# Performance work log

Hardware: AMD Instinct MI355X
Metric: run time of the kernel (lower is better)

The kernel has to match this reference:

```python
import jax, jax.numpy as jnp
import numpy as np

D_MODEL = 1024
N_HEADS = 16
HEAD_DIM = D_MODEL // N_HEADS
D_FF = 4096
SEQ = 2048
BATCH = 4
THETA = 10000.0
EPS = 1e-5


def rmsnorm(x, w, eps=EPS):
    xf = x.astype(jnp.float32)
    var = jnp.mean(xf * xf, axis=-1, keepdims=True) + eps
    return (xf * jax.lax.rsqrt(var) * w).astype(x.dtype)


def rope_tables(head_dim, max_len, theta):
    freqs = 1.0 / theta ** (jnp.arange(0, head_dim, 2, dtype=jnp.float32) / head_dim)
    t = jnp.arange(max_len, dtype=jnp.float32)
    ang = jnp.outer(t, freqs)  # [T, Hs/2]
    return jnp.cos(ang), jnp.sin(ang)


def apply_rope(x, cos, sin):
    # x: [B, H, T, Hs]; cos/sin: [T, Hs/2] (broadcast over B, H)
    x1 = x[..., 0::2]
    x2 = x[..., 1::2]
    o1 = x1 * cos - x2 * sin
    o2 = x1 * sin + x2 * cos
    return jnp.stack([o1, o2], axis=-1).reshape(x.shape).astype(x.dtype)


def setup_inputs() -> dict:
    key = jax.random.key(0)
    ks = jax.random.split(key, 12)
    s = 0.02
    return {
        "x": jax.random.normal(ks[0], (BATCH, SEQ, D_MODEL), dtype=jnp.float32),
        "token_positions": jnp.arange(SEQ, dtype=jnp.int32),
        "ln1_w": jnp.ones((D_MODEL,), dtype=jnp.float32),
        "q_w": jax.random.normal(ks[1], (D_MODEL, D_MODEL), dtype=jnp.float32) * s,
        "k_w": jax.random.normal(ks[2], (D_MODEL, D_MODEL), dtype=jnp.float32) * s,
        "v_w": jax.random.normal(ks[3], (D_MODEL, D_MODEL), dtype=jnp.float32) * s,
        "o_w": jax.random.normal(ks[4], (D_MODEL, D_MODEL), dtype=jnp.float32) * s,
        "ln2_w": jnp.ones((D_MODEL,), dtype=jnp.float32),
        "w1": jax.random.normal(ks[5], (D_FF, D_MODEL), dtype=jnp.float32) * s,
        "w2": jax.random.normal(ks[6], (D_MODEL, D_FF), dtype=jnp.float32) * s,
        "w3": jax.random.normal(ks[7], (D_FF, D_MODEL), dtype=jnp.float32) * s,
    }


def reference(x, token_positions, ln1_w, q_w, k_w, v_w, o_w, ln2_w, w1, w2, w3):
    B, T, D = x.shape
    cos_full, sin_full = rope_tables(HEAD_DIM, SEQ, THETA)
    cos = cos_full[token_positions]
    sin = sin_full[token_positions]

    # --- attention sublayer ---
    h = rmsnorm(x, ln1_w)
    q = jnp.einsum('btd,od->bto', h, q_w)
    k = jnp.einsum('btd,od->bto', h, k_w)
    v = jnp.einsum('btd,od->bto', h, v_w)
    # [B, T, D] -> [B, H, T, Hs]
    def split_heads(t_):
        return t_.reshape(B, T, N_HEADS, HEAD_DIM).transpose(0, 2, 1, 3)
    xq, xk, xv = split_heads(q), split_heads(k), split_heads(v)
    xq = apply_rope(xq, cos, sin)
    xk = apply_rope(xk, cos, sin)

    scores = jnp.einsum('bhqd,bhkd->bhqk', xq, xk) / jnp.sqrt(jnp.float32(HEAD_DIM))
    causal = jnp.tril(jnp.ones((T, T), dtype=bool))
    scores = jnp.where(causal, scores, jnp.float32(-jnp.inf))
    attn = jax.nn.softmax(scores, axis=-1)
    ctx = jnp.einsum('bhqk,bhkd->bhqd', attn, xv)
    ctx = ctx.transpose(0, 2, 1, 3).reshape(B, T, D)
    x = x + jnp.einsum('btd,od->bto', ctx, o_w)

    # --- SwiGLU FFN sublayer ---
    h2 = rmsnorm(x, ln2_w)
    a = jnp.einsum('btd,fd->btf', h2, w1)
    g = jnp.einsum('btd,fd->btf', h2, w3)
    ff = jnp.einsum('btf,df->btd', a * jax.nn.sigmoid(a) * g, w2)
    return x + ff
```

## Files before the change

### kernel.cpp

```cpp
#include <hip/hip_runtime.h>
#include <hip/hip_bf16.h>

#define D_MODEL 1024
#define N_HEADS 16
#define HEAD_DIM 64
#define D_FF 4096
#define SEQ 2048
#define BATCH 4
#define NTOK (BATCH*SEQ)

typedef __attribute__((ext_vector_type(4))) float  f32x4;
typedef __attribute__((ext_vector_type(8))) short  s16x8;
typedef __attribute__((ext_vector_type(4))) unsigned short u16x4;

typedef __attribute__((address_space(1))) const unsigned int gas_u32;
typedef __attribute__((address_space(3))) unsigned int las_u32;

__device__ __forceinline__ void gload_lds16(const void* g, void* l) {
  __builtin_amdgcn_global_load_lds((gas_u32*)g, (las_u32*)l, 16, 0, 0);
}

__device__ __forceinline__ float bf2f(unsigned short u) {
  union { unsigned int i; float f; } v; v.i = ((unsigned int)u) << 16; return v.f;
}
__device__ __forceinline__ unsigned short f2bf(float f) {
  union { float f; unsigned int i; } v; v.f = f;
  return (unsigned short)((v.i + 0x7fffu + ((v.i >> 16) & 1u)) >> 16);
}

__global__ __launch_bounds__(256) void cvt_k(const float* __restrict__ in,
                                             unsigned short* __restrict__ out, int n) {
  for (long i = ((long)blockIdx.x*256 + threadIdx.x)*4; i < n; i += (long)gridDim.x*1024) {
    f32x4 v = *(const f32x4*)&in[i];
    u16x4 o;
    #pragma unroll
    for (int c=0;c<4;c++) o[c] = f2bf(v[c]);
    *(u16x4*)&out[i] = o;
  }
}

__global__ __launch_bounds__(256) void rope_tables_k(const int* __restrict__ pos,
                                                     float* __restrict__ cosT,
                                                     float* __restrict__ sinT) {
  int idx = blockIdx.x*256 + threadIdx.x;
  int t = idx >> 5, i = idx & 31;
  float p  = (float)pos[t];
  float fr = powf(10000.0f, -(float)i * (1.0f/32.0f));
  float ang = p * fr;
  cosT[idx] = cosf(ang);
  sinT[idx] = sinf(ang);
}

__global__ __launch_bounds__(256) void rmsnorm_k(const float* __restrict__ x,
                                                 const float* __restrict__ wgt,
                                                 unsigned short* __restrict__ out) {
  const long row = blockIdx.x;
  const int t = threadIdx.x;
  f32x4 v = *(const f32x4*)&x[row*D_MODEL + t*4];
  float ss = v[0]*v[0] + v[1]*v[1] + v[2]*v[2] + v[3]*v[3];
  #pragma unroll
  for (int off=1; off<64; off<<=1) ss += __shfl_xor(ss, off, 64);
  __shared__ float red[4];
  if ((t & 63) == 0) red[t >> 6] = ss;
  __syncthreads();
  float tot = red[0] + red[1] + red[2] + red[3];
  float inv = rsqrtf(tot * (1.0f/D_MODEL) + 1e-5f);
  f32x4 wv = *(const f32x4*)&wgt[t*4];
  u16x4 o;
  #pragma unroll
  for (int c=0;c<4;c++) o[c] = f2bf(v[c] * inv * wv[c]);
  *(u16x4*)&out[row*D_MODEL + t*4] = o;
}

__global__ __launch_bounds__(256) void rope_k(unsigned short* __restrict__ q,
                                              unsigned short* __restrict__ k,
                                              const float* __restrict__ cosT,
                                              const float* __restrict__ sinT) {
  long idx = (long)blockIdx.x*256 + threadIdx.x;
  int ig = (int)(idx & 7);
  long th = idx >> 3;
  int h = (int)(th & 15);
  long bt = th >> 4;
  int t = (int)(bt & (SEQ-1));
  long off = bt*D_MODEL + h*HEAD_DIM + ig*8;
  f32x4 cs = *(const f32x4*)&cosT[t*32 + ig*4];
  f32x4 sn = *(const f32x4*)&sinT[t*32 + ig*4];
  s16x8 qv = *(const s16x8*)&q[off];
  s16x8 kv = *(const s16x8*)&k[off];
  s16x8 qo, ko;
  #pragma unroll
  for (int p=0;p<4;p++) {
    float q1 = bf2f((unsigned short)qv[2*p]), q2 = bf2f((unsigned short)qv[2*p+1]);
    qo[2*p]   = (short)f2bf(q1*cs[p] - q2*sn[p]);
    qo[2*p+1] = (short)f2bf(q1*sn[p] + q2*cs[p]);
    float k1 = bf2f((unsigned short)kv[2*p]), k2 = bf2f((unsigned short)kv[2*p+1]);
    ko[2*p]   = (short)f2bf(k1*cs[p] - k2*sn[p]);
    ko[2*p+1] = (short)f2bf(k1*sn[p] + k2*cs[p]);
  }
  *(s16x8*)&q[off] = qo;
  *(s16x8*)&k[off] = ko;
}

template<int EPI>
__global__ __launch_bounds__(256) void gemm_bt(const unsigned short* __restrict__ A,
                                               const unsigned short* __restrict__ W,
                                               unsigned short* __restrict__ Cb,
                                               float* __restrict__ Cf,
                                               const float* __restrict__ resid,
                                               int M, int N, int K) {
  __shared__ __align__(16) unsigned short As[128*64];
  __shared__ __align__(16) unsigned short Bs[128*64];

  const int nwg = gridDim.x * gridDim.y;
  int orig = blockIdx.y * gridDim.x + blockIdx.x;
  int swz = orig;
  if ((nwg & 7) == 0) {
    int cpx = nwg >> 3;
    swz = (orig & 7) * cpx + (orig >> 3);
  }
  const int bx = swz % gridDim.x;
  const int by = swz / gridDim.x;

  const int tid = threadIdx.x;
  const int w  = tid >> 6;
  const int l  = tid & 63;
  const int lr = l & 15;
  const int lg = l >> 4;
  const int wm = (w >> 1) * 64;
  const int wn = (w & 1) * 64;

  const long rowA0 = (long)by * 128;
  const long rowB0 = (long)bx * 128;

  f32x4 acc[4][4] = {};

  for (int kt = 0; kt < K; kt += 64) {
    #pragma unroll
    for (int it = 0; it < 4; ++it) {
      int chunk = it*256 + tid;
      int row = chunk >> 3;
      int csw = (chunk & 7) ^ (row & 7);
      gload_lds16(&A[(rowA0 + row)*(long)K + kt + csw*8], &As[chunk*8]);
    }
    #pragma unroll
    for (int it = 0; it < 4; ++it) {
      int chunk = it*256 + tid;
      int row = chunk >> 3;
      int csw = (chunk & 7) ^ (row & 7);
      gload_lds16(&W[(rowB0 + row)*(long)K + kt + csw*8], &Bs[chunk*8]);
    }
    __syncthreads();

    s16x8 af[2][4], bfv[2][4];
    #pragma unroll
    for (int m=0;m<4;m++) {
      int row = wm + m*16 + lr;
      #pragma unroll
      for (int kk=0;kk<2;kk++) {
        int sw = (kk*4+lg) ^ (row & 7);
        af[kk][m] = *(const s16x8*)&As[row*64 + sw*8];
      }
    }
    #pragma unroll
    for (int n=0;n<4;n++) {
      int row = wn + n*16 + lr;
      #pragma unroll
      for (int kk=0;kk<2;kk++) {
        int sw = (kk*4+lg) ^ (row & 7);
        bfv[kk][n] = *(const s16x8*)&Bs[row*64 + sw*8];
      }
    }
    #pragma unroll
    for (int kk=0;kk<2;kk++)
      #pragma unroll
      for (int m=0;m<4;m++)
        #pragma unroll
        for (int n=0;n<4;n++)
          acc[m][n] = __builtin_amdgcn_mfma_f32_16x16x32_bf16(af[kk][m], bfv[kk][n], acc[m][n], 0,0,0);
    __syncthreads();
  }

  #pragma unroll
  for (int m=0;m<4;m++)
    #pragma unroll
    for (int n=0;n<4;n++)
      #pragma unroll
      for (int r=0;r<4;r++) {
        long row = rowA0 + wm + m*16 + lg*4 + r;
        long col = rowB0 + wn + n*16 + lr;
        float val = acc[m][n][r];
        if constexpr (EPI == 0) {
          Cb[row*(long)N + col] = f2bf(val);
        } else {
          Cf[row*(long)N + col] = resid[row*(long)N + col] + val;
        }
      }
}

__global__ __launch_bounds__(256) void attn_k(const unsigned short* __restrict__ Q,
                                              const unsigned short* __restrict__ K,
                                              const unsigned short* __restrict__ V,
                                              unsigned short* __restrict__ O) {
  const int bh = blockIdx.x;
  const int b = bh >> 4;
  const int h = bh & 15;
  const int tid = threadIdx.x;
  const int w  = tid >> 6;
  const int l  = tid & 63;
  const int lr = l & 15;
  const int lg = l >> 4;

  __shared__ __align__(16) unsigned short Vs[2][64*64];
  __shared__ __align__(16) unsigned short Ps[4][16][72];

  const int skv = tid >> 2;
  const int sd0 = (tid & 3) * 16;
  const long vbase = (long)(b*SEQ)*D_MODEL + h*HEAD_DIM;

  for (int pass = 0; pass < 2; ++pass) {
    const int qt = pass ? 31 - blockIdx.y : blockIdx.y;
    const int q0 = qt * 64;
    const int ntile = qt + 1;

    const long rowQ = (long)(b*SEQ + q0 + w*16 + lr);
    s16x8 qf0 = *(const s16x8*)&Q[rowQ*D_MODEL + h*HEAD_DIM + lg*8];
    s16x8 qf1 = *(const s16x8*)&Q[rowQ*D_MODEL + h*HEAD_DIM + 32 + lg*8];

    float mi[4], li[4];
    f32x4 oa[4] = {};
    #pragma unroll
    for (int r=0;r<4;r++) { mi[r] = -1e30f; li[r] = 0.f; }

    {
      const unsigned short* src = &V[vbase + (long)skv*D_MODEL + sd0];
      s16x8 v0 = *(const s16x8*)&src[0];
      s16x8 v1 = *(const s16x8*)&src[8];
      #pragma unroll
      for (int i=0;i<16;i++) {
        int d = sd0 + i;
        int key = (d&7) ^ ((d>>3)&7);
        int c = (skv>>3) ^ key;
        Vs[0][d*64 + c*8 + (skv&7)] = (unsigned short)(i<8 ? v0[i] : v1[i-8]);
      }
    }
    __syncthreads();

    for (int t=0; t<ntile; ++t) {
      const int kv0 = t*64;
      const int cur = t & 1;
      const int nb  = cur ^ 1;
      const bool more = (t+1 < ntile);

      s16x8 v0, v1;
      if (more) {
        const unsigned short* src = &V[vbase + (long)((t+1)*64 + skv)*D_MODEL + sd0];
        v0 = *(const s16x8*)&src[0];
        v1 = *(const s16x8*)&src[8];
      }

      f32x4 s[4];
      #pragma unroll
      for (int j=0;j<4;j++) {
        const long rowK = (long)(b*SEQ + kv0 + j*16 + lr);
        s16x8 kf0 = *(const s16x8*)&K[rowK*D_MODEL + h*HEAD_DIM + lg*8];
        s16x8 kf1 = *(const s16x8*)&K[rowK*D_MODEL + h*HEAD_DIM + 32 + lg*8];
        f32x4 acc = {};
        acc = __builtin_amdgcn_mfma_f32_16x16x32_bf16(qf0, kf0, acc, 0,0,0);
        acc = __builtin_amdgcn_mfma_f32_16x16x32_bf16(qf1, kf1, acc, 0,0,0);
        s[j] = acc * 0.125f;
      }
      if (t == ntile-1) {
        #pragma unroll
        for (int j=0;j<4;j++)
          #pragma unroll
          for (int r=0;r<4;r++) {
            int kvg = kv0 + j*16 + lr;
            int qg  = q0 + w*16 + lg*4 + r;
            if (kvg > qg) s[j][r] = -1e30f;
          }
      }
      float al[4];
      #pragma unroll
      for (int r=0;r<4;r++) {
        float v = fmaxf(fmaxf(s[0][r], s[1][r]), fmaxf(s[2][r], s[3][r]));
        #pragma unroll
        for (int off=1; off<16; off<<=1) v = fmaxf(v, __shfl_xor(v, off, 64));
        float mn = fmaxf(mi[r], v);
        al[r] = __expf(mi[r] - mn);
        mi[r] = mn;
      }
      #pragma unroll
      for (int j=0;j<4;j++)
        #pragma unroll
        for (int r=0;r<4;r++) s[j][r] = __expf(s[j][r] - mi[r]);
      #pragma unroll
      for (int r=0;r<4;r++) {
        float v = s[0][r]+s[1][r]+s[2][r]+s[3][r];
        #pragma unroll
        for (int off=1; off<16; off<<=1) v += __shfl_xor(v, off, 64);
        li[r] = li[r]*al[r] + v;
      }
      #pragma unroll
      for (int d=0;d<4;d++)
        #pragma unroll
        for (int r=0;r<4;r++) oa[d][r] *= al[r];
      #pragma unroll
      for (int j=0;j<4;j++)
        #pragma unroll
        for (int r=0;r<4;r++)
          Ps[w][lg*4+r][j*16+lr] = f2bf(s[j][r]);

      if (more) {
        #pragma unroll
        for (int i=0;i<16;i++) {
          int d = sd0 + i;
          int key = (d&7) ^ ((d>>3)&7);
          int c = (skv>>3) ^ key;
          Vs[nb][d*64 + c*8 + (skv&7)] = (unsigned short)(i<8 ? v0[i] : v1[i-8]);
        }
      }

      #pragma unroll
      for (int kk=0;kk<2;kk++) {
        s16x8 pa = *(const s16x8*)&Ps[w][lr][kk*32+lg*8];
        #pragma unroll
        for (int d=0;d<4;d++) {
          int row = d*16 + lr;
          int key = (row&7) ^ ((row>>3)&7);
          int c = (kk*4+lg) ^ key;
          s16x8 vb = *(const s16x8*)&Vs[cur][row*64 + c*8];
          oa[d] = __builtin_amdgcn_mfma_f32_16x16x32_bf16(pa, vb, oa[d], 0,0,0);
        }
      }
      __syncthreads();
    }

    #pragma unroll
    for (int d=0;d<4;d++)
      #pragma unroll
      for (int r=0;r<4;r++) {
        long row = (long)(b*SEQ + q0 + w*16 + lg*4 + r);
        O[row*D_MODEL + h*HEAD_DIM + d*16 + lr] = f2bf(oa[d][r] / li[r]);
      }
  }
}

__global__ __launch_bounds__(256) void swiglu_k(unsigned short* __restrict__ a,
                                                const unsigned short* __restrict__ g) {
  long i = ((long)blockIdx.x*256 + threadIdx.x)*8;
  s16x8 av = *(const s16x8*)&a[i];
  s16x8 gv = *(const s16x8*)&g[i];
  s16x8 o;
  #pragma unroll
  for (int c=0;c<8;c++) {
    float xx = bf2f((unsigned short)av[c]);
    float yy = bf2f((unsigned short)gv[c]);
    float sg = 1.0f / (1.0f + __expf(-xx));
    o[c] = (short)f2bf(xx * sg * yy);
  }
  *(s16x8*)&a[i] = o;
}

extern "C" void kernel_launch(void* const* d_in, const int* in_sizes, int n_in,
                              void* d_out, int out_size, void* d_ws, size_t ws_size,
                              hipStream_t stream) {
  (void)in_sizes; (void)n_in; (void)out_size; (void)ws_size;
  const float* x    = (const float*)d_in[0];
  const int*   tpos = (const int*)d_in[1];
  const float* ln1  = (const float*)d_in[2];
  const float* qw   = (const float*)d_in[3];
  const float* kw   = (const float*)d_in[4];
  const float* vw   = (const float*)d_in[5];
  const float* ow   = (const float*)d_in[6];
  const float* ln2  = (const float*)d_in[7];
  const float* w1   = (const float*)d_in[8];
  const float* w2   = (const float*)d_in[9];
  const float* w3   = (const float*)d_in[10];
  float* out = (float*)d_out;

  char* ws = (char*)d_ws;
  size_t off = 0;
  auto nalloc = [&](size_t b) { void* p = ws + off; off += (b + 255) & ~(size_t)255; return p; };

  unsigned short* wqb = (unsigned short*)nalloc((size_t)D_MODEL*D_MODEL*2);
  unsigned short* wkb = (unsigned short*)nalloc((size_t)D_MODEL*D_MODEL*2);
  unsigned short* wvb = (unsigned short*)nalloc((size_t)D_MODEL*D_MODEL*2);
  unsigned short* wob = (unsigned short*)nalloc((size_t)D_MODEL*D_MODEL*2);
  unsigned short* w1b = (unsigned short*)nalloc((size_t)D_FF*D_MODEL*2);
  unsigned short* w3b = (unsigned short*)nalloc((size_t)D_FF*D_MODEL*2);
  unsigned short* w2b = (unsigned short*)nalloc((size_t)D_MODEL*D_FF*2);
  float* cosT = (float*)nalloc((size_t)SEQ*32*4);
  float* sinT = (float*)nalloc((size_t)SEQ*32*4);
  unsigned short* h    = (unsigned short*)nalloc((size_t)NTOK*D_MODEL*2);
  unsigned short* qb   = (unsigned short*)nalloc((size_t)NTOK*D_MODEL*2);
  unsigned short* kb   = (unsigned short*)nalloc((size_t)NTOK*D_MODEL*2);
  unsigned short* vb   = (unsigned short*)nalloc((size_t)NTOK*D_MODEL*2);
  unsigned short* ctxb = (unsigned short*)nalloc((size_t)NTOK*D_MODEL*2);
  float* x2 = (float*)nalloc((size_t)NTOK*D_MODEL*4);
  unsigned short* gbuf = (unsigned short*)nalloc((size_t)NTOK*D_FF*2);
  unsigned short* abuf = qb;

  cvt_k<<<1024,256,0,stream>>>(qw, wqb, D_MODEL*D_MODEL);
  cvt_k<<<1024,256,0,stream>>>(kw, wkb, D_MODEL*D_MODEL);
  cvt_k<<<1024,256,0,stream>>>(vw, wvb, D_MODEL*D_MODEL);
  cvt_k<<<1024,256,0,stream>>>(ow, wob, D_MODEL*D_MODEL);
  cvt_k<<<2048,256,0,stream>>>(w1, w1b, D_FF*D_MODEL);
  cvt_k<<<2048,256,0,stream>>>(w2, w2b, D_MODEL*D_FF);
  cvt_k<<<2048,256,0,stream>>>(w3, w3b, D_FF*D_MODEL);
  rope_tables_k<<<SEQ*32/256,256,0,stream>>>(tpos, cosT, sinT);

  rmsnorm_k<<<NTOK,256,0,stream>>>(x, ln1, h);
  gemm_bt<0><<<dim3(8,64),256,0,stream>>>(h, wqb, qb, nullptr, nullptr, NTOK, D_MODEL, D_MODEL);
  gemm_bt<0><<<dim3(8,64),256,0,stream>>>(h, wkb, kb, nullptr, nullptr, NTOK, D_MODEL, D_MODEL);
  gemm_bt<0><<<dim3(8,64),256,0,stream>>>(h, wvb, vb, nullptr, nullptr, NTOK, D_MODEL, D_MODEL);
  rope_k<<<4096,256,0,stream>>>(qb, kb, cosT, sinT);
  attn_k<<<dim3(64,16),256,0,stream>>>(qb, kb, vb, ctxb);
  gemm_bt<1><<<dim3(8,64),256,0,stream>>>(ctxb, wob, nullptr, x2, x, NTOK, D_MODEL, D_MODEL);

  rmsnorm_k<<<NTOK,256,0,stream>>>(x2, ln2, h);
  gemm_bt<0><<<dim3(32,64),256,0,stream>>>(h, w1b, abuf, nullptr, nullptr, NTOK, D_FF, D_MODEL);
  gemm_bt<0><<<dim3(32,64),256,0,stream>>>(h, w3b, gbuf, nullptr, nullptr, NTOK, D_FF, D_MODEL);
  swiglu_k<<<(long)NTOK*D_FF/8/256,256,0,stream>>>(abuf, gbuf);
  gemm_bt<1><<<dim3(8,64),256,0,stream>>>(abuf, w2b, nullptr, out, x2, NTOK, D_MODEL, D_FF);
}
```

Measured before the change: 719.2 us.

## Fuse QKV projection, stage K in LDS, restructure attention softmax, add double-buffered GEMM

Packs Q, K and V weights into one matrix so a single GEMM writes an interleaved QKV buffer, replacing three launches. RoPE now also folds the 1/sqrt(d) scale into Q. The attention kernel loads K tiles into swizzled, double-buffered LDS and computes the transposed score product so softmax reductions need fewer shuffles. It also swizzles the P buffer and raises wave priority around MFMA sections. A new double-buffered gemm_db kernel is introduced but used only for the w1 projection, and it doubles LDS use, which may lower occupancy.

After: 647.1 us. -10.0%, faster.

```diff
diff --git a/kernel.cpp b/kernel.cpp
--- a/kernel.cpp
+++ b/kernel.cpp
@@ -8,6 +8,7 @@
 #define SEQ 2048
 #define BATCH 4
 #define NTOK (BATCH*SEQ)
+#define QS 3072
 
 typedef __attribute__((ext_vector_type(4))) float  f32x4;
 typedef __attribute__((ext_vector_type(8))) short  s16x8;
@@ -72,8 +73,7 @@
   *(u16x4*)&out[row*D_MODEL + t*4] = o;
 }
 
-__global__ __launch_bounds__(256) void rope_k(unsigned short* __restrict__ q,
-                                              unsigned short* __restrict__ k,
+__global__ __launch_bounds__(256) void rope_k(unsigned short* __restrict__ qkv,
                                               const float* __restrict__ cosT,
                                               const float* __restrict__ sinT) {
   long idx = (long)blockIdx.x*256 + threadIdx.x;
@@ -82,23 +82,23 @@
   int h = (int)(th & 15);
   long bt = th >> 4;
   int t = (int)(bt & (SEQ-1));
-  long off = bt*D_MODEL + h*HEAD_DIM + ig*8;
+  long off = bt*QS + h*HEAD_DIM + ig*8;
   f32x4 cs = *(const f32x4*)&cosT[t*32 + ig*4];
   f32x4 sn = *(const f32x4*)&sinT[t*32 + ig*4];
-  s16x8 qv = *(const s16x8*)&q[off];
-  s16x8 kv = *(const s16x8*)&k[off];
+  s16x8 qv = *(const s16x8*)&qkv[off];
+  s16x8 kv = *(const s16x8*)&qkv[off + 1024];
   s16x8 qo, ko;
   #pragma unroll
   for (int p=0;p<4;p++) {
     float q1 = bf2f((unsigned short)qv[2*p]), q2 = bf2f((unsigned short)qv[2*p+1]);
-    qo[2*p]   = (short)f2bf(q1*cs[p] - q2*sn[p]);
-    qo[2*p+1] = (short)f2bf(q1*sn[p] + q2*cs[p]);
+    qo[2*p]   = (short)f2bf((q1*cs[p] - q2*sn[p]) * 0.125f);
+    qo[2*p+1] = (short)f2bf((q1*sn[p] + q2*cs[p]) * 0.125f);
     float k1 = bf2f((unsigned short)kv[2*p]), k2 = bf2f((unsigned short)kv[2*p+1]);
     ko[2*p]   = (short)f2bf(k1*cs[p] - k2*sn[p]);
     ko[2*p+1] = (short)f2bf(k1*sn[p] + k2*cs[p]);
   }
-  *(s16x8*)&q[off] = qo;
-  *(s16x8*)&k[off] = ko;
+  *(s16x8*)&qkv[off] = qo;
+  *(s16x8*)&qkv[off + 1024] = ko;
 }
 
 template<int EPI>
@@ -197,9 +197,111 @@
       }
 }
 
-__global__ __launch_bounds__(256) void attn_k(const unsigned short* __restrict__ Q,
-                                              const unsigned short* __restrict__ K,
-                                              const unsigned short* __restrict__ V,
+template<int EPI>
+__global__ __launch_bounds__(256) void gemm_db(const unsigned short* __restrict__ A,
+                                               const unsigned short* __restrict__ W,
+                                               unsigned short* __restrict__ Cb,
+                                               float* __restrict__ Cf,
+                                               const float* __restrict__ resid,
+                                               int M, int N, int K) {
+  __shared__ __align__(16) unsigned short As[2][128*64];
+  __shared__ __align__(16) unsigned short Bs[2][128*64];
+
+  const int nwg = gridDim.x * gridDim.y;
+  int orig = blockIdx.y * gridDim.x + blockIdx.x;
+  int swz = orig;
+  if ((nwg & 7) == 0) {
+    int cpx = nwg >> 3;
+    swz = (orig & 7) * cpx + (orig >> 3);
+  }
+  const int bx = swz % gridDim.x;
+  const int by = swz / gridDim.x;
+
+  const int tid = threadIdx.x;
+  const int w  = tid >> 6;
+  const int l  = tid & 63;
+  const int lr = l & 15;
+  const int lg = l >> 4;
+  const int wm = (w >> 1) * 64;
+  const int wn = (w & 1) * 64;
+
+  const long rowA0 = (long)by * 128;
+  const long rowB0 = (long)bx * 128;
+
+  f32x4 acc[4][4] = {};
+  const int nk = K >> 6;
+
+  #pragma unroll
+  for (int it = 0; it < 4; ++it) {
+    int chunk = it*256 + tid;
+    int row = chunk >> 3;
+    int csw = (chunk & 7) ^ (row & 7);
+    gload_lds16(&A[(rowA0 + row)*(long)K + csw*8], &As[0][chunk*8]);
+    gload_lds16(&W[(rowB0 + row)*(long)K + csw*8], &Bs[0][chunk*8]);
+  }
+  __syncthreads();
+
+  int cur = 0;
+  for (int ki = 0; ki < nk; ++ki) {
+    if (ki + 1 < nk) {
+      int kt = (ki + 1) << 6;
+      #pragma unroll
+      for (int it = 0; it < 4; ++it) {
+        int chunk = it*256 + tid;
+        int row = chunk >> 3;
+        int csw = (chunk & 7) ^ (row & 7);
+        gload_lds16(&A[(rowA0 + row)*(long)K + kt + csw*8], &As[cur^1][chunk*8]);
+        gload_lds16(&W[(rowB0 + row)*(long)K + kt + csw*8], &Bs[cur^1][chunk*8]);
+      }
+    }
+    s16x8 af[2][4], bfv[2][4];
+    #pragma unroll
+    for (int m=0;m<4;m++) {
+      int row = wm + m*16 + lr;
+      #pragma unroll
+      for (int kk=0;kk<2;kk++) {
+        int sw = (kk*4+lg) ^ (row & 7);
+        af[kk][m] = *(const s16x8*)&As[cur][row*64 + sw*8];
+      }
+    }
+    #pragma unroll
+    for (int n=0;n<4;n++) {
+      int row = wn + n*16 + lr;
+      #pragma unroll
+      for (int kk=0;kk<2;kk++) {
+        int sw = (kk*4+lg) ^ (row & 7);
+        bfv[kk][n] = *(const s16x8*)&Bs[cur][row*64 + sw*8];
+      }
+    }
+    #pragma unroll
+    for (int kk=0;kk<2;kk++)
+      #pragma unroll
+      for (int m=0;m<4;m++)
+        #pragma unroll
+        for (int n=0;n<4;n++)
+          acc[m][n] = __builtin_amdgcn_mfma_f32_16x16x32_bf16(af[kk][m], bfv[kk][n], acc[m][n], 0,0,0);
+    __syncthreads();
+    cur ^= 1;
+  }
+
+  #pragma unroll
+  for (int m=0;m<4;m++)
+    #pragma unroll
+    for (int n=0;n<4;n++)
+      #pragma unroll
+      for (int r=0;r<4;r++) {
+        long row = rowA0 + wm + m*16 + lg*4 + r;
+        long col = rowB0 + wn + n*16 + lr;
+        float val = acc[m][n][r];
+        if constexpr (EPI == 0) {
+          Cb[row*(long)N + col] = f2bf(val);
+        } else {
+          Cf[row*(long)N + col] = resid[row*(long)N + col] + val;
+        }
+      }
+}
+
+__global__ __launch_bounds__(256) void attn_k(const unsigned short* __restrict__ QKV,
                                               unsigned short* __restrict__ O) {
   const int bh = blockIdx.x;
   const int b = bh >> 4;
@@ -210,29 +312,39 @@
   const int lr = l & 15;
   const int lg = l >> 4;
 
+  const unsigned short* Qp = QKV;
+  const unsigned short* Kp = QKV + 1024;
+  const unsigned short* Vp = QKV + 2048;
+
+  __shared__ __align__(16) unsigned short Ks[2][64*64];
   __shared__ __align__(16) unsigned short Vs[2][64*64];
-  __shared__ __align__(16) unsigned short Ps[4][16][72];
+  __shared__ __align__(16) unsigned short Ps[4][16][64];
 
   const int skv = tid >> 2;
   const int sd0 = (tid & 3) * 16;
-  const long vbase = (long)(b*SEQ)*D_MODEL + h*HEAD_DIM;
+  const long hbase = (long)(b*SEQ)*QS + h*HEAD_DIM;
 
   for (int pass = 0; pass < 2; ++pass) {
-    const int qt = pass ? 31 - blockIdx.y : blockIdx.y;
+    const int qt = pass ? 31 - (int)blockIdx.y : (int)blockIdx.y;
     const int q0 = qt * 64;
     const int ntile = qt + 1;
 
     const long rowQ = (long)(b*SEQ + q0 + w*16 + lr);
-    s16x8 qf0 = *(const s16x8*)&Q[rowQ*D_MODEL + h*HEAD_DIM + lg*8];
-    s16x8 qf1 = *(const s16x8*)&Q[rowQ*D_MODEL + h*HEAD_DIM + 32 + lg*8];
-
-    float mi[4], li[4];
+    s16x8 qf0 = *(const s16x8*)&Qp[rowQ*QS + h*HEAD_DIM + lg*8];
+    s16x8 qf1 = *(const s16x8*)&Qp[rowQ*QS + h*HEAD_DIM + 32 + lg*8];
+
+    float mi = -1e30f, li = 0.f;
     f32x4 oa[4] = {};
-    #pragma unroll
-    for (int r=0;r<4;r++) { mi[r] = -1e30f; li[r] = 0.f; }
-
+
+    #pragma unroll
+    for (int it=0; it<2; ++it) {
+      int chunk = it*256 + tid;
+      int row = chunk >> 3;
+      int csw = (chunk & 7) ^ (row & 7);
+      gload_lds16(&Kp[hbase + (long)row*QS + csw*8], &Ks[0][chunk*8]);
+    }
     {
-      const unsigned short* src = &V[vbase + (long)skv*D_MODEL + sd0];
+      const unsigned short* src = &Vp[hbase + (long)skv*QS + sd0];
       s16x8 v0 = *(const s16x8*)&src[0];
       s16x8 v1 = *(const s16x8*)&src[8];
       #pragma unroll
@@ -253,62 +365,79 @@
 
       s16x8 v0, v1;
       if (more) {
-        const unsigned short* src = &V[vbase + (long)((t+1)*64 + skv)*D_MODEL + sd0];
+        #pragma unroll
+        for (int it=0; it<2; ++it) {
+          int chunk = it*256 + tid;
+          int row = chunk >> 3;
+          int csw = (chunk & 7) ^ (row & 7);
+          gload_lds16(&Kp[hbase + (long)(kv0 + 64 + row)*QS + csw*8], &Ks[nb][chunk*8]);
+        }
+        const unsigned short* src = &Vp[hbase + (long)(kv0 + 64 + skv)*QS + sd0];
         v0 = *(const s16x8*)&src[0];
         v1 = *(const s16x8*)&src[8];
       }
 
       f32x4 s[4];
+      __builtin_amdgcn_s_setprio(1);
       #pragma unroll
       for (int j=0;j<4;j++) {
-        const long rowK = (long)(b*SEQ + kv0 + j*16 + lr);
-        s16x8 kf0 = *(const s16x8*)&K[rowK*D_MODEL + h*HEAD_DIM + lg*8];
-        s16x8 kf1 = *(const s16x8*)&K[rowK*D_MODEL + h*HEAD_DIM + 32 + lg*8];
+        int krow = j*16 + lr;
+        s16x8 kf0 = *(const s16x8*)&Ks[cur][krow*64 + ((lg)     ^ (krow&7))*8];
+        s16x8 kf1 = *(const s16x8*)&Ks[cur][krow*64 + ((4 + lg) ^ (krow&7))*8];
         f32x4 acc = {};
-        acc = __builtin_amdgcn_mfma_f32_16x16x32_bf16(qf0, kf0, acc, 0,0,0);
-        acc = __builtin_amdgcn_mfma_f32_16x16x32_bf16(qf1, kf1, acc, 0,0,0);
-        s[j] = acc * 0.125f;
-      }
+        acc = __builtin_amdgcn_mfma_f32_16x16x32_bf16(kf0, qf0, acc, 0,0,0);
+        acc = __builtin_amdgcn_mfma_f32_16x16x32_bf16(kf1, qf1, acc, 0,0,0);
+        s[j] = acc;
+      }
+      __builtin_amdgcn_s_setprio(0);
+
       if (t == ntile-1) {
         #pragma unroll
         for (int j=0;j<4;j++)
           #pragma unroll
-          for (int r=0;r<4;r++) {
-            int kvg = kv0 + j*16 + lr;
-            int qg  = q0 + w*16 + lg*4 + r;
-            if (kvg > qg) s[j][r] = -1e30f;
-          }
-      }
-      float al[4];
-      #pragma unroll
-      for (int r=0;r<4;r++) {
-        float v = fmaxf(fmaxf(s[0][r], s[1][r]), fmaxf(s[2][r], s[3][r]));
-        #pragma unroll
-        for (int off=1; off<16; off<<=1) v = fmaxf(v, __shfl_xor(v, off, 64));
-        float mn = fmaxf(mi[r], v);
-        al[r] = __expf(mi[r] - mn);
-        mi[r] = mn;
-      }
+          for (int r=0;r<4;r++)
+            if (kv0 + j*16 + lg*4 + r > q0 + w*16 + lr) s[j][r] = -1e30f;
+      }
+
+      float pmax = s[0][0];
       #pragma unroll
       for (int j=0;j<4;j++)
         #pragma unroll
-        for (int r=0;r<4;r++) s[j][r] = __expf(s[j][r] - mi[r]);
-      #pragma unroll
-      for (int r=0;r<4;r++) {
-        float v = s[0][r]+s[1][r]+s[2][r]+s[3][r];
-        #pragma unroll
-        for (int off=1; off<16; off<<=1) v += __shfl_xor(v, off, 64);
-        li[r] = li[r]*al[r] + v;
-      }
+        for (int r=0;r<4;r++) pmax = fmaxf(pmax, s[j][r]);
+      pmax = fmaxf(pmax, __shfl_xor(pmax, 16, 64));
+      pmax = fmaxf(pmax, __shfl_xor(pmax, 32, 64));
+      float mn = fmaxf(mi, pmax);
+      float al = __expf(mi - mn);
+      mi = mn;
+      float psum = 0.f;
+      #pragma unroll
+      for (int j=0;j<4;j++)
+        #pragma unroll
+        for (int r=0;r<4;r++) {
+          float p = __expf(s[j][r] - mn);
+          s[j][r] = p;
+          psum += p;
+        }
+      psum += __shfl_xor(psum, 16, 64);
+      psum += __shfl_xor(psum, 32, 64);
+      li = li*al + psum;
+
+      float alq[4];
+      #pragma unroll
+      for (int r=0;r<4;r++) alq[r] = __shfl(al, lg*4 + r, 64);
       #pragma unroll
       for (int d=0;d<4;d++)
         #pragma unroll
-        for (int r=0;r<4;r++) oa[d][r] *= al[r];
+        for (int r=0;r<4;r++) oa[d][r] *= alq[r];
+
       #pragma unroll
       for (int j=0;j<4;j++)
         #pragma unroll
-        for (int r=0;r<4;r++)
-          Ps[w][lg*4+r][j*16+lr] = f2bf(s[j][r]);
+        for (int r=0;r<4;r++) {
+          int k = j*16 + lg*4 + r;
+          int pos = ((k>>3) ^ (lr&7))*8 + (k&7);
+          Ps[w][lr][pos] = f2bf(s[j][r]);
+        }
 
       if (more) {
         #pragma unroll
@@ -320,27 +449,32 @@
         }
       }
 
+      __builtin_amdgcn_s_setprio(1);
       #pragma unroll
       for (int kk=0;kk<2;kk++) {
-        s16x8 pa = *(const s16x8*)&Ps[w][lr][kk*32+lg*8];
+        s16x8 pa = *(const s16x8*)&Ps[w][lr][((kk*4 + lg) ^ (lr&7))*8];
         #pragma unroll
         for (int d=0;d<4;d++) {
-          int row = d*16 + lr;
-          int key = (row&7) ^ ((row>>3)&7);
-          int c = (kk*4+lg) ^ key;
-          s16x8 vb = *(const s16x8*)&Vs[cur][row*64 + c*8];
+          int vrow = d*16 + lr;
+          int key = (vrow&7) ^ ((vrow>>3)&7);
+          int c = (kk*4 + lg) ^ key;
+          s16x8 vb = *(const s16x8*)&Vs[cur][vrow*64 + c*8];
           oa[d] = __builtin_amdgcn_mfma_f32_16x16x32_bf16(pa, vb, oa[d], 0,0,0);
         }
       }
+      __builtin_amdgcn_s_setprio(0);
       __syncthreads();
     }
 
+    float liq[4];
+    #pragma unroll
+    for (int r=0;r<4;r++) liq[r] = __shfl(li, lg*4 + r, 64);
     #pragma unroll
     for (int d=0;d<4;d++)
       #pragma unroll
       for (int r=0;r<4;r++) {
         long row = (long)(b*SEQ + q0 + w*16 + lg*4 + r);
-        O[row*D_MODEL + h*HEAD_DIM + d*16 + lr] = f2bf(oa[d][r] / li[r]);
+        O[row*D_MODEL + h*HEAD_DIM + d*16 + lr] = f2bf(oa[d][r] / liq[r]);
       }
   }
 }
@@ -382,44 +516,38 @@
   size_t off = 0;
   auto nalloc = [&](size_t b) { void* p = ws + off; off += (b + 255) & ~(size_t)255; return p; };
 
-  unsigned short* wqb = (unsigned short*)nalloc((size_t)D_MODEL*D_MODEL*2);
-  unsigned short* wkb = (unsigned short*)nalloc((size_t)D_MODEL*D_MODEL*2);
-  unsigned short* wvb = (unsigned short*)nalloc((size_t)D_MODEL*D_MODEL*2);
-  unsigned short* wob = (unsigned short*)nalloc((size_t)D_MODEL*D_MODEL*2);
-  unsigned short* w1b = (unsigned short*)nalloc((size_t)D_FF*D_MODEL*2);
-  unsigned short* w3b = (unsigned short*)nalloc((size_t)D_FF*D_MODEL*2);
-  unsigned short* w2b = (unsigned short*)nalloc((size_t)D_MODEL*D_FF*2);
+  unsigned short* wqkvb = (unsigned short*)nalloc((size_t)3072*D_MODEL*2);
+  unsigned short* wob   = (unsigned short*)nalloc((size_t)D_MODEL*D_MODEL*2);
+  unsigned short* w1b   = (unsigned short*)nalloc((size_t)D_FF*D_MODEL*2);
+  unsigned short* w3b   = (unsigned short*)nalloc((size_t)D_FF*D_MODEL*2);
+  unsigned short* w2b   = (unsigned short*)nalloc((size_t)D_MODEL*D_FF*2);
   float* cosT = (float*)nalloc((size_t)SEQ*32*4);
   float* sinT = (float*)nalloc((size_t)SEQ*32*4);
-  unsigned short* h    = (unsigned short*)nalloc((size_t)NTOK*D_MODEL*2);
-  unsigned short* qb   = (unsigned short*)nalloc((size_t)NTOK*D_MODEL*2);
-  unsigned short* kb   = (unsigned short*)nalloc((size_t)NTOK*D_MODEL*2);
-  unsigned short* vb   = (unsigned short*)nalloc((size_t)NTOK*D_MODEL*2);
+  unsigned short* hbuf = (unsigned short*)nalloc((size_t)NTOK*D_MODEL*2);
+  unsigned short* qkv  = (unsigned short*)nalloc((size_t)NTOK*QS*2);
   unsigned short* ctxb = (unsigned short*)nalloc((size_t)NTOK*D_MODEL*2);
   float* x2 = (float*)nalloc((size_t)NTOK*D_MODEL*4);
   unsigned short* gbuf = (unsigned short*)nalloc((size_t)NTOK*D_FF*2);
-  unsigned short* abuf = qb;
-
-  cvt_k<<<1024,256,0,stream>>>(qw, wqb, D_MODEL*D_MODEL);
-  cvt_k<<<1024,256,0,stream>>>(kw, wkb, D_MODEL*D_MODEL);
-  cvt_k<<<1024,256,0,stream>>>(vw, wvb, D_MODEL*D_MODEL);
+  unsigned short* abuf = qkv;
+
+  cvt_k<<<1024,256,0,stream>>>(qw, wqkvb,                 D_MODEL*D_MODEL);
+  cvt_k<<<1024,256,0,stream>>>(kw, wqkvb + 1024*D_MODEL,  D_MODEL*D_MODEL);
+  cvt_k<<<1024,256,0,stream>>>(vw, wqkvb + 2048*D_MODEL,  D_MODEL*D_MODEL);
   cvt_k<<<1024,256,0,stream>>>(ow, wob, D_MODEL*D_MODEL);
   cvt_k<<<2048,256,0,stream>>>(w1, w1b, D_FF*D_MODEL);
   cvt_k<<<2048,256,0,stream>>>(w2, w2b, D_MODEL*D_FF);
   cvt_k<<<2048,256,0,stream>>>(w3, w3b, D_FF*D_MODEL);
   rope_tables_k<<<SEQ*32/256,256,0,stream>>>(tpos, cosT, sinT);
 
-  rmsnorm_k<<<NTOK,256,0,stream>>>(x, ln1, h);
-  gemm_bt<0><<<dim3(8,64),256,0,stream>>>(h, wqb, qb, nullptr, nullptr, NTOK, D_MODEL, D_MODEL);
-  gemm_bt<0><<<dim3(8,64),256,0,stream>>>(h, wkb, kb, nullptr, nullptr, NTOK, D_MODEL, D_MODEL);
-  gemm_bt<0><<<dim3(8,64),256,0,stream>>>(h, wvb, vb, nullptr, nullptr, NTOK, D_MODEL, D_MODEL);
-  rope_k<<<4096,256,0,stream>>>(qb, kb, cosT, sinT);
-  attn_k<<<dim3(64,16),256,0,stream>>>(qb, kb, vb, ctxb);
+  rmsnorm_k<<<NTOK,256,0,stream>>>(x, ln1, hbuf);
+  gemm_bt<0><<<dim3(24,64),256,0,stream>>>(hbuf, wqkvb, qkv, nullptr, nullptr, NTOK, QS, D_MODEL);
+  rope_k<<<4096,256,0,stream>>>(qkv, cosT, sinT);
+  attn_k<<<dim3(64,16),256,0,stream>>>(qkv, ctxb);
   gemm_bt<1><<<dim3(8,64),256,0,stream>>>(ctxb, wob, nullptr, x2, x, NTOK, D_MODEL, D_MODEL);
 
-  rmsnorm_k<<<NTOK,256,0,stream>>>(x2, ln2, h);
-  gemm_bt<0><<<dim3(32,64),256,0,stream>>>(h, w1b, abuf, nullptr, nullptr, NTOK, D_FF, D_MODEL);
-  gemm_bt<0><<<dim3(32,64),256,0,stream>>>(h, w3b, gbuf, nullptr, nullptr, NTOK, D_FF, D_MODEL);
+  rmsnorm_k<<<NTOK,256,0,stream>>>(x2, ln2, hbuf);
+  gemm_db<0><<<dim3(32,64),256,0,stream>>>(hbuf, w1b, abuf, nullptr, nullptr, NTOK, D_FF, D_MODEL);
+  gemm_bt<0><<<dim3(32,64),256,0,stream>>>(hbuf, w3b, gbuf, nullptr, nullptr, NTOK, D_FF, D_MODEL);
   swiglu_k<<<(long)NTOK*D_FF/8/256,256,0,stream>>>(abuf, gbuf);
   gemm_bt<1><<<dim3(8,64),256,0,stream>>>(abuf, w2b, nullptr, out, x2, NTOK, D_MODEL, D_FF);
 }
```
